# Kernel tuning notes

Hardware: AMD Instinct MI355X
Metric: run time of the kernel (lower is better)

## Reference

```python
import jax, jax.numpy as jnp
import numpy as np

K = 10        # neighbors kept (after dropping self)
N_SEEDS = 20  # FPS seeds
H = 0.01      # repulsion bandwidth


def setup_inputs() -> dict:
    key = jax.random.key(0)
    pcs = jax.random.uniform(key, (16, 65536, 3), dtype=jnp.float32)
    return {"pcs": pcs}


def farthest_point_sample(xyz, npoint, key):
    """Iterative FPS. xyz: [B,N,C] -> centroids [B,npoint] (int)."""
    B, N, C = xyz.shape
    distance = jnp.full((B, N), 1e10, dtype=xyz.dtype)
    farthest = jax.random.randint(key, (B,), 0, N)
    bidx = jnp.arange(B)

    def step(carry, _):
        dist_min, far = carry
        centroid = xyz[bidx, far][:, None, :]              # [B,1,C]
        d = jnp.sum((xyz - centroid) ** 2, axis=-1)        # [B,N]
        dist_min = jnp.minimum(dist_min, d)
        return (dist_min, jnp.argmax(dist_min, axis=-1)), far

    _, cents = jax.lax.scan(step, (distance, farthest), None, length=npoint)
    return cents.T  # [B, npoint]


def reference(pcs):
    B, N, C = pcs.shape
    seeds = farthest_point_sample(pcs, N_SEEDS, jax.random.key(1))   # [B,S]
    seeds_value = jnp.take_along_axis(
        pcs, jnp.broadcast_to(seeds[:, :, None], (B, N_SEEDS, C)), axis=1
    )  # [B,S,3]
    diff = pcs[:, :, None, :] - seeds_value[:, None, :, :]           # [B,N,S,3]
    sq = jnp.sum(diff * diff, axis=-1)                               # [B,N,S]
    # safe L2 norm (exact zeros at seed-vs-itself)
    dist = jnp.where(sq == 0, 0.0, jnp.sqrt(jnp.where(sq == 0, 1.0, sq)))
    dist_sn = dist.transpose(0, 2, 1)                                # [B,S,N]
    # k+1 smallest distances per seed, ascending (torch.topk largest=False)
    neg_top, _ = jax.lax.top_k(-dist_sn, K + 1)                      # [B,S,K+1]
    top_dist_net = -neg_top[:, :, 1:]                                # drop self, [B,S,K]
    weights = jnp.exp(-(top_dist_net ** 2) / (H * H))
    repulsion = -top_dist_net * weights
    return repulsion.sum(axis=2).sum(axis=1).mean()
```

## Files before the change

### kernel.cpp

```cpp
#include <hip/hip_runtime.h>
#include <cstdint>
#include <cfloat>
#include <cmath>

#define NPTS 65536
#define NB 16
#define NS 20
#define KK 10
#define FPB 8
#define PPT 8
#define NSm1 (NS - 1)

struct InitIdx { int idx[NB]; };

static __device__ __forceinline__ unsigned long long
agent_ld(const unsigned long long* p) {
    return __hip_atomic_load(p, __ATOMIC_RELAXED, __HIP_MEMORY_SCOPE_AGENT);
}

__global__ __launch_bounds__(1024) void fps_kernel(const float* __restrict__ pcs,
                                                   int* __restrict__ seeds,
                                                   unsigned long long* __restrict__ fkey,
                                                   InitIdx init) {
    const int u   = blockIdx.x;
    const int xcd = u & 7;
    const int k   = u >> 3;
    const int b   = 2 * xcd + (k >> 3);
    const int j   = k & 7;
    const int t   = threadIdx.x;
    const int lane = t & 63;
    const int w    = t >> 6;
    const float* __restrict__ base = pcs + (size_t)b * NPTS * 3;
    const int pbase = j * 8192 + t * 8;

    float x[PPT], y[PPT], z[PPT], dm[PPT];
    {
        const float4* q4 = reinterpret_cast<const float4*>(base + (size_t)pbase * 3);
#pragma unroll
        for (int g = 0; g < 2; ++g) {
            float4 A = q4[g * 3 + 0], Bv = q4[g * 3 + 1], Cv = q4[g * 3 + 2];
            x[g*4+0] = A.x;  y[g*4+0] = A.y;  z[g*4+0] = A.z;
            x[g*4+1] = A.w;  y[g*4+1] = Bv.x; z[g*4+1] = Bv.y;
            x[g*4+2] = Bv.z; y[g*4+2] = Bv.w; z[g*4+2] = Cv.x;
            x[g*4+3] = Cv.y; y[g*4+3] = Cv.z; z[g*4+3] = Cv.w;
        }
#pragma unroll
        for (int q = 0; q < PPT; ++q) dm[q] = 1e10f;
    }

    __shared__ float s_val[16];
    __shared__ int   s_idx[16];
    __shared__ int   s_far;

    int far = init.idx[b];

    for (int s = 0; s < NS; ++s) {
        if (j == 0 && t == 0) seeds[b * NS + s] = far;
        if (s == NSm1) break;

        const float* c = base + (size_t)far * 3;
        const float cx = c[0], cy = c[1], cz = c[2];

        float bestv = -1.0f;
        int   besti = 0;
#pragma unroll
        for (int q = 0; q < PPT; ++q) {
            float dx = __fsub_rn(x[q], cx);
            float dy = __fsub_rn(y[q], cy);
            float dz = __fsub_rn(z[q], cz);
            float d  = __fadd_rn(__fadd_rn(__fmul_rn(dx, dx), __fmul_rn(dy, dy)),
                                 __fmul_rn(dz, dz));
            dm[q] = fminf(dm[q], d);
            if (dm[q] > bestv) { bestv = dm[q]; besti = pbase + q; }
        }
#pragma unroll
        for (int off = 32; off >= 1; off >>= 1) {
            float ov = __shfl_down(bestv, off);
            int   oi = __shfl_down(besti, off);
            if (ov > bestv || (ov == bestv && oi < besti)) { bestv = ov; besti = oi; }
        }
        if (lane == 0) { s_val[w] = bestv; s_idx[w] = besti; }
        __syncthreads();

        if (w == 0) {
            unsigned long long kv = 0ULL;
            if (lane < 16) {
                kv = ((unsigned long long)__float_as_uint(s_val[lane]) << 32) |
                     (unsigned long long)(0xFFFFFFFFu - (unsigned int)s_idx[lane]);
            }
#pragma unroll
            for (int off = 8; off >= 1; off >>= 1) {
                unsigned int lo = (unsigned int)kv, hi = (unsigned int)(kv >> 32);
                unsigned int olo = (unsigned int)__shfl_xor((int)lo, off);
                unsigned int ohi = (unsigned int)__shfl_xor((int)hi, off);
                unsigned long long o = ((unsigned long long)ohi << 32) | olo;
                if (o > kv) kv = o;
            }
            unsigned long long* fp = fkey + (size_t)(b * NS + s) * FPB;
            if (lane == 0)
                __hip_atomic_store(&fp[j], kv, __ATOMIC_RELAXED,
                                   __HIP_MEMORY_SCOPE_AGENT);

            const unsigned long long* sl = fp + (lane & 7);
            unsigned long long p0 = agent_ld(sl);
            unsigned long long p1 = agent_ld(sl);
            unsigned long long p2 = agent_ld(sl);
            unsigned long long v;
            for (;;) {
                if (!__any(p0 == 0ULL)) { v = p0; break; }
                p0 = agent_ld(sl);
                if (!__any(p1 == 0ULL)) { v = p1; break; }
                p1 = agent_ld(sl);
                if (!__any(p2 == 0ULL)) { v = p2; break; }
                p2 = agent_ld(sl);
            }
#pragma unroll
            for (int off = 32; off >= 1; off >>= 1) {
                unsigned int lo = (unsigned int)v, hi = (unsigned int)(v >> 32);
                unsigned int olo = (unsigned int)__shfl_xor((int)lo, off);
                unsigned int ohi = (unsigned int)__shfl_xor((int)hi, off);
                unsigned long long o = ((unsigned long long)ohi << 32) | olo;
                if (o > v) v = o;
            }
            if (lane == 0)
                s_far = (int)(0xFFFFFFFFu - (unsigned int)(v & 0xFFFFFFFFull));
        }
        __syncthreads();
        far = s_far;
    }
}

__global__ __launch_bounds__(256) void knn_scan(const float* __restrict__ pcs,
                                                const int* __restrict__ seeds,
                                                float* __restrict__ part) {
    const int u   = blockIdx.x;
    const int xcd = u & 7;
    const int k   = u >> 3;
    const int b   = 2 * xcd + (k / 80);
    const int rem = k % 80;
    const int s   = rem >> 2;
    const int c   = rem & 3;
    const int t = threadIdx.x;
    const int lane = t & 63;
    const int w = t >> 6;
    const float* __restrict__ base = pcs + (size_t)b * NPTS * 3;
    const int sidx = seeds[b * NS + s];
    const float cx = base[(size_t)sidx * 3 + 0];
    const float cy = base[(size_t)sidx * 3 + 1];
    const float cz = base[(size_t)sidx * 3 + 2];

    float lst[11];
#pragma unroll
    for (int jj = 0; jj < 11; ++jj) lst[jj] = FLT_MAX;

    for (int i = 0; i < 16; ++i) {
        const int pbase = c * 16384 + i * 1024 + t * 4;
        const float4* q4 = reinterpret_cast<const float4*>(base + (size_t)pbase * 3);
        float4 A = q4[0], Bv = q4[1], Cv = q4[2];
        float px[4] = { A.x, A.w, Bv.z, Cv.y };
        float py[4] = { A.y, Bv.x, Bv.w, Cv.z };
        float pz[4] = { A.z, Bv.y, Cv.x, Cv.w };
#pragma unroll
        for (int q = 0; q < 4; ++q) {
            float dx = __fsub_rn(px[q], cx);
            float dy = __fsub_rn(py[q], cy);
            float dz = __fsub_rn(pz[q], cz);
            float sq = __fadd_rn(__fadd_rn(__fmul_rn(dx, dx), __fmul_rn(dy, dy)),
                                 __fmul_rn(dz, dz));
#pragma unroll
            for (int jj = 10; jj >= 1; --jj)
                lst[jj] = __builtin_amdgcn_fmed3f(lst[jj - 1], lst[jj], sq);
            lst[0] = fminf(lst[0], sq);
        }
    }

    float* pr = part + ((size_t)((b * NS + s) * 4 + c) * 4 + w) * 11;
    for (int r = 0; r < 11; ++r) {
        float v = lst[0];
#pragma unroll
        for (int off = 32; off >= 1; off >>= 1) v = fminf(v, __shfl_xor(v, off));
        unsigned long long m = __ballot(lst[0] == v);
        if (lane == (int)__ffsll(m) - 1) {
#pragma unroll
            for (int jj = 0; jj < 10; ++jj) lst[jj] = lst[jj + 1];
            lst[10] = FLT_MAX;
        }
        if (lane == 0) pr[r] = v;
    }
}

__global__ __launch_bounds__(64) void knn_merge(const float* __restrict__ part,
                                                float* __restrict__ out) {
    const int pair = blockIdx.x;
    const int lane = threadIdx.x;
    const float* flat = part + (size_t)pair * 176;
    float a0 = flat[lane];
    float a1 = flat[lane + 64];
    float a2 = (lane + 128 < 176) ? flat[lane + 128] : FLT_MAX;

    const float HH = (float)(0.01 * 0.01);
    float acc = 0.0f;
#pragma unroll
    for (int r = 0; r < 11; ++r) {
        float mymin = fminf(a0, fminf(a1, a2));
        float v = mymin;
#pragma unroll
        for (int off = 32; off >= 1; off >>= 1) v = fminf(v, __shfl_xor(v, off));
        unsigned long long m = __ballot(mymin == v);
        if (lane == (int)__ffsll(m) - 1) {
            if (a0 == v)      a0 = FLT_MAX;
            else if (a1 == v) a1 = FLT_MAX;
            else              a2 = FLT_MAX;
        }
        if (lane == 0 && r >= 1) {
            float sq = v;
            float d  = (sq == 0.0f) ? 0.0f : __fsqrt_rn(sq);
            float q2 = __fmul_rn(d, d);
            float wt = expf(__fdiv_rn(-q2, HH));
            acc = __fadd_rn(acc, -__fmul_rn(d, wt));
        }
    }
    if (lane == 0) atomicAdd(out, acc * 0.0625f);
}

static inline uint32_t rotl32(uint32_t x, uint32_t d) { return (x << d) | (x >> (32 - d)); }

static void tf2x32(uint32_t k0, uint32_t k1, uint32_t x0, uint32_t x1,
                   uint32_t& y0, uint32_t& y1) {
    const uint32_t ks[3] = { k0, k1, k0 ^ k1 ^ 0x1BD11BDAu };
    const uint32_t rotA[4] = { 13, 15, 26, 6 };
    const uint32_t rotB[4] = { 17, 29, 16, 24 };
    uint32_t v0 = x0 + ks[0], v1 = x1 + ks[1];
    for (int i = 0; i < 5; ++i) {
        const uint32_t* rot = (i % 2 == 0) ? rotA : rotB;
        for (int j = 0; j < 4; ++j) {
            v0 += v1;
            v1 = rotl32(v1, rot[j]);
            v1 ^= v0;
        }
        v0 += ks[(i + 1) % 3];
        v1 += ks[(i + 2) % 3] + (uint32_t)(i + 1);
    }
    y0 = v0; y1 = v1;
}

extern "C" void kernel_launch(void* const* d_in, const int* in_sizes, int n_in,
                              void* d_out, int out_size, void* d_ws, size_t ws_size,
                              hipStream_t stream) {
    const float* pcs = (const float*)d_in[0];
    float* out = (float*)d_out;

    int* seeds               = (int*)d_ws;
    unsigned long long* fkey = (unsigned long long*)((char*)d_ws + 2048);
    float* part              = (float*)((char*)d_ws + 24576);

    uint32_t k2_0, k2_1;
    tf2x32(0u, 1u, 0u, 1u, k2_0, k2_1);
    InitIdx init;
    for (int i = 0; i < NB; ++i) {
        uint32_t y0, y1;
        tf2x32(k2_0, k2_1, 0u, (uint32_t)i, y0, y1);
        init.idx[i] = (int)((y0 ^ y1) & 0xFFFFu);
    }

    hipMemsetAsync(d_ws, 0, 22528, stream);
    hipMemsetAsync(d_out, 0, sizeof(float), stream);

    hipLaunchKernelGGL(fps_kernel, dim3(NB * FPB), dim3(1024), 0, stream,
                       pcs, seeds, fkey, init);
    hipLaunchKernelGGL(knn_scan, dim3(1280), dim3(256), 0, stream,
                       pcs, seeds, part);
    hipLaunchKernelGGL(knn_merge, dim3(320), dim3(64), 0, stream,
                       part, out);
}
```

Measured before the change: 81.83 us.

## Spread FPS across more blocks and add independent top-k lists with prefetch in kNN scan

The FPS kernel now uses 16 blocks per batch, each holding 4 points per thread instead of 8 blocks with 8 points. This halves the per-step compute per block but doubles the number of partial keys each block must poll on the cross-block exchange. The kNN scan keeps four independent 11-element insertion lists per thread to break the serial fmed3 dependency chain, and prefetches the next tile's points. This raises register pressure, so it adds a launch-bounds occupancy hint and merges the four lists during extraction. Workspace offsets and the memset size are adjusted for the larger key buffer.

```diff
diff --git a/kernel.cpp b/kernel.cpp
--- a/kernel.cpp
+++ b/kernel.cpp
@@ -7,8 +7,7 @@
 #define NB 16
 #define NS 20
 #define KK 10
-#define FPB 8
-#define PPT 8
+#define FPB 16
 #define NSm1 (NS - 1)
 
 struct InitIdx { int idx[NB]; };
@@ -25,28 +24,20 @@
     const int u   = blockIdx.x;
     const int xcd = u & 7;
     const int k   = u >> 3;
-    const int b   = 2 * xcd + (k >> 3);
-    const int j   = k & 7;
+    const int b   = 2 * xcd + (k >> 4);
+    const int j   = k & 15;
     const int t   = threadIdx.x;
     const int lane = t & 63;
     const int w    = t >> 6;
     const float* __restrict__ base = pcs + (size_t)b * NPTS * 3;
-    const int pbase = j * 8192 + t * 8;
-
-    float x[PPT], y[PPT], z[PPT], dm[PPT];
-    {
-        const float4* q4 = reinterpret_cast<const float4*>(base + (size_t)pbase * 3);
-#pragma unroll
-        for (int g = 0; g < 2; ++g) {
-            float4 A = q4[g * 3 + 0], Bv = q4[g * 3 + 1], Cv = q4[g * 3 + 2];
-            x[g*4+0] = A.x;  y[g*4+0] = A.y;  z[g*4+0] = A.z;
-            x[g*4+1] = A.w;  y[g*4+1] = Bv.x; z[g*4+1] = Bv.y;
-            x[g*4+2] = Bv.z; y[g*4+2] = Bv.w; z[g*4+2] = Cv.x;
-            x[g*4+3] = Cv.y; y[g*4+3] = Cv.z; z[g*4+3] = Cv.w;
-        }
-#pragma unroll
-        for (int q = 0; q < PPT; ++q) dm[q] = 1e10f;
-    }
+    const int pbase = j * 4096 + t * 4;
+
+    const float4* q4 = reinterpret_cast<const float4*>(base + (size_t)pbase * 3);
+    float4 A = q4[0], Bv = q4[1], Cv = q4[2];
+    float x[4] = { A.x, A.w, Bv.z, Cv.y };
+    float y[4] = { A.y, Bv.x, Bv.w, Cv.z };
+    float z[4] = { A.z, Bv.y, Cv.x, Cv.w };
+    float dm[4] = { 1e10f, 1e10f, 1e10f, 1e10f };
 
     __shared__ float s_val[16];
     __shared__ int   s_idx[16];
@@ -64,7 +55,7 @@
         float bestv = -1.0f;
         int   besti = 0;
 #pragma unroll
-        for (int q = 0; q < PPT; ++q) {
+        for (int q = 0; q < 4; ++q) {
             float dx = __fsub_rn(x[q], cx);
             float dy = __fsub_rn(y[q], cy);
             float dz = __fsub_rn(z[q], cz);
@@ -101,7 +92,7 @@
                 __hip_atomic_store(&fp[j], kv, __ATOMIC_RELAXED,
                                    __HIP_MEMORY_SCOPE_AGENT);
 
-            const unsigned long long* sl = fp + (lane & 7);
+            const unsigned long long* sl = fp + (lane & 15);
             unsigned long long p0 = agent_ld(sl);
             unsigned long long p1 = agent_ld(sl);
             unsigned long long p2 = agent_ld(sl);
@@ -130,9 +121,17 @@
     }
 }
 
-__global__ __launch_bounds__(256) void knn_scan(const float* __restrict__ pcs,
-                                                const int* __restrict__ seeds,
-                                                float* __restrict__ part) {
+#define INS11(L, SQ)                                                     \
+    {                                                                    \
+        _Pragma("unroll")                                                \
+        for (int jj = 10; jj >= 1; --jj)                                 \
+            L[jj] = __builtin_amdgcn_fmed3f(L[jj - 1], L[jj], (SQ));     \
+        L[0] = fminf(L[0], (SQ));                                        \
+    }
+
+__global__ __launch_bounds__(256, 5) void knn_scan(const float* __restrict__ pcs,
+                                                   const int* __restrict__ seeds,
+                                                   float* __restrict__ part) {
     const int u   = blockIdx.x;
     const int xcd = u & 7;
     const int k   = u >> 3;
@@ -149,48 +148,75 @@
     const float cy = base[(size_t)sidx * 3 + 1];
     const float cz = base[(size_t)sidx * 3 + 2];
 
-    float lst[11];
-#pragma unroll
-    for (int jj = 0; jj < 11; ++jj) lst[jj] = FLT_MAX;
+    float l0[11], l1[11], l2[11], l3[11];
+#pragma unroll
+    for (int jj = 0; jj < 11; ++jj) { l0[jj] = FLT_MAX; l1[jj] = FLT_MAX;
+                                      l2[jj] = FLT_MAX; l3[jj] = FLT_MAX; }
+
+    const float4* qp = reinterpret_cast<const float4*>(
+        base + (size_t)(c * 16384 + t * 4) * 3);
+    float4 A = qp[0], Bv = qp[1], Cv = qp[2];
 
     for (int i = 0; i < 16; ++i) {
-        const int pbase = c * 16384 + i * 1024 + t * 4;
-        const float4* q4 = reinterpret_cast<const float4*>(base + (size_t)pbase * 3);
-        float4 A = q4[0], Bv = q4[1], Cv = q4[2];
-        float px[4] = { A.x, A.w, Bv.z, Cv.y };
-        float py[4] = { A.y, Bv.x, Bv.w, Cv.z };
-        float pz[4] = { A.z, Bv.y, Cv.x, Cv.w };
-#pragma unroll
-        for (int q = 0; q < 4; ++q) {
-            float dx = __fsub_rn(px[q], cx);
-            float dy = __fsub_rn(py[q], cy);
-            float dz = __fsub_rn(pz[q], cz);
-            float sq = __fadd_rn(__fadd_rn(__fmul_rn(dx, dx), __fmul_rn(dy, dy)),
-                                 __fmul_rn(dz, dz));
-#pragma unroll
-            for (int jj = 10; jj >= 1; --jj)
-                lst[jj] = __builtin_amdgcn_fmed3f(lst[jj - 1], lst[jj], sq);
-            lst[0] = fminf(lst[0], sq);
-        }
+        float4 nA, nB, nC;
+        if (i < 15) {
+            const float4* np = reinterpret_cast<const float4*>(
+                base + (size_t)(c * 16384 + (i + 1) * 1024 + t * 4) * 3);
+            nA = np[0]; nB = np[1]; nC = np[2];
+        }
+        const float px0 = A.x,  py0 = A.y,  pz0 = A.z;
+        const float px1 = A.w,  py1 = Bv.x, pz1 = Bv.y;
+        const float px2 = Bv.z, py2 = Bv.w, pz2 = Cv.x;
+        const float px3 = Cv.y, py3 = Cv.z, pz3 = Cv.w;
+
+        {   float dx = __fsub_rn(px0, cx), dy = __fsub_rn(py0, cy), dz = __fsub_rn(pz0, cz);
+            float sq = __fadd_rn(__fadd_rn(__fmul_rn(dx, dx), __fmul_rn(dy, dy)), __fmul_rn(dz, dz));
+            INS11(l0, sq); }
+        {   float dx = __fsub_rn(px1, cx), dy = __fsub_rn(py1, cy), dz = __fsub_rn(pz1, cz);
+            float sq = __fadd_rn(__fadd_rn(__fmul_rn(dx, dx), __fmul_rn(dy, dy)), __fmul_rn(dz, dz));
+            INS11(l1, sq); }
+        {   float dx = __fsub_rn(px2, cx), dy = __fsub_rn(py2, cy), dz = __fsub_rn(pz2, cz);
+            float sq = __fadd_rn(__fadd_rn(__fmul_rn(dx, dx), __fmul_rn(dy, dy)), __fmul_rn(dz, dz));
+            INS11(l2, sq); }
+        {   float dx = __fsub_rn(px3, cx), dy = __fsub_rn(py3, cy), dz = __fsub_rn(pz3, cz);
+            float sq = __fadd_rn(__fadd_rn(__fmul_rn(dx, dx), __fmul_rn(dy, dy)), __fmul_rn(dz, dz));
+            INS11(l3, sq); }
+
+        A = nA; Bv = nB; Cv = nC;
     }
 
     float* pr = part + ((size_t)((b * NS + s) * 4 + c) * 4 + w) * 11;
     for (int r = 0; r < 11; ++r) {
-        float v = lst[0];
+        float h = fminf(fminf(l0[0], l1[0]), fminf(l2[0], l3[0]));
+        float v = h;
 #pragma unroll
         for (int off = 32; off >= 1; off >>= 1) v = fminf(v, __shfl_xor(v, off));
-        unsigned long long m = __ballot(lst[0] == v);
+        unsigned long long m = __ballot(h == v);
         if (lane == (int)__ffsll(m) - 1) {
-#pragma unroll
-            for (int jj = 0; jj < 10; ++jj) lst[jj] = lst[jj + 1];
-            lst[10] = FLT_MAX;
+            if (l0[0] == v) {
+#pragma unroll
+                for (int jj = 0; jj < 10; ++jj) l0[jj] = l0[jj + 1];
+                l0[10] = FLT_MAX;
+            } else if (l1[0] == v) {
+#pragma unroll
+                for (int jj = 0; jj < 10; ++jj) l1[jj] = l1[jj + 1];
+                l1[10] = FLT_MAX;
+            } else if (l2[0] == v) {
+#pragma unroll
+                for (int jj = 0; jj < 10; ++jj) l2[jj] = l2[jj + 1];
+                l2[10] = FLT_MAX;
+            } else {
+#pragma unroll
+                for (int jj = 0; jj < 10; ++jj) l3[jj] = l3[jj + 1];
+                l3[10] = FLT_MAX;
+            }
         }
         if (lane == 0) pr[r] = v;
     }
 }
 
 __global__ __launch_bounds__(64) void knn_merge(const float* __restrict__ part,
-                                                float* __restrict__ out) {
+                                               float* __restrict__ out) {
     const int pair = blockIdx.x;
     const int lane = threadIdx.x;
     const float* flat = part + (size_t)pair * 176;
@@ -252,7 +278,7 @@
 
     int* seeds               = (int*)d_ws;
     unsigned long long* fkey = (unsigned long long*)((char*)d_ws + 2048);
-    float* part              = (float*)((char*)d_ws + 24576);
+    float* part              = (float*)((char*)d_ws + 49152);
 
     uint32_t k2_0, k2_1;
     tf2x32(0u, 1u, 0u, 1u, k2_0, k2_1);
@@ -263,7 +289,7 @@
         init.idx[i] = (int)((y0 ^ y1) & 0xFFFFu);
     }
 
-    hipMemsetAsync(d_ws, 0, 22528, stream);
+    hipMemsetAsync(d_ws, 0, 43008, stream);
     hipMemsetAsync(d_out, 0, sizeof(float), stream);
 
     hipLaunchKernelGGL(fps_kernel, dim3(NB * FPB), dim3(1024), 0, stream,
```

Measured after the change: 110.1 us. 1.35x slower.
